# Kernel tuning notes

Hardware: AMD Instinct MI355X
Metric: run time of the kernel (lower is better)

The kernel has to match this reference:

```python
import jax, jax.numpy as jnp
import numpy as np
import math

B, LQ, LK = 4, 512, 512
D_MODEL, NHEAD, NLABELS = 512, 8, 8
D_Q = D_MODEL // NHEAD


def setup_inputs() -> dict:
    key = jax.random.key(0)
    ks = jax.random.split(key, 12)
    xavier = lambda k, shape: jax.random.uniform(
        k, shape, jnp.float32,
        -math.sqrt(6.0 / (shape[0] + shape[1])), math.sqrt(6.0 / (shape[0] + shape[1])))
    return {
        "q": jax.random.normal(ks[0], (B, LQ, D_MODEL), jnp.float32),
        "k": jax.random.normal(ks[1], (B, LK, D_MODEL), jnp.float32),
        "edge_mask": jax.random.randint(ks[2], (B, LQ, LK, NLABELS), 0, 2).astype(jnp.float32),
        "padding_mask": jax.random.randint(ks[3], (B, LQ, LK), 0, 2).astype(jnp.float32),
        "w_q_w": xavier(ks[4], (D_MODEL, D_MODEL)),
        "w_q_b": jnp.zeros((D_MODEL,), jnp.float32),
        "w_k": xavier(ks[5], (D_MODEL, D_MODEL)),
        "w_v": xavier(ks[6], (D_MODEL, D_MODEL)),
        "w_h_w": xavier(ks[7], (D_MODEL, D_MODEL)),
        "w_h_b": jnp.zeros((D_MODEL,), jnp.float32),
        "b_ks": xavier(ks[8], (NLABELS, D_Q)),
        "b_vs": xavier(ks[9], (NLABELS, D_Q)),
    }


def reference(q, k, edge_mask, padding_mask, w_q_w, w_q_b, w_k, w_v, w_h_w, w_h_b, b_ks, b_vs):
    sz_b, len_q, _ = q.shape
    len_k = k.shape[1]
    temp = np.power(D_Q, 0.5).astype(np.float32)

    # projections -> (nhead, B, L, d_q), matching torch permute(2,0,1,3)
    query = (q @ w_q_w.T + w_q_b).reshape(sz_b, len_q, NHEAD, D_Q).transpose(2, 0, 1, 3)
    key = (k @ w_k.T).reshape(sz_b, len_k, NHEAD, D_Q).transpose(2, 0, 1, 3)
    value = (k @ w_v.T).reshape(sz_b, len_k, NHEAD, D_Q).transpose(2, 0, 1, 3)

    # content scores + relation-bias scores
    qk = jnp.einsum('hbqd,hbkd->hbqk', query, key)
    key_rel = jnp.einsum('bqkl,ld->bqkd', edge_mask, b_ks)      # (B,Lq,Lk,d_q)
    qkr = jnp.einsum('hbqd,bqkd->hbqk', query, key_rel)
    output_attention_weights = (qk + qkr) / temp                # pre-mask, as returned by torch

    # mask where no edge label AND padding_mask==1
    relation_mask = (edge_mask.sum(-1) + (1.0 - padding_mask)) == 0  # (B,Lq,Lk)
    rm = relation_mask[None, :, :, :]                                # broadcast over heads
    attn = jnp.where(rm, -jnp.inf, output_attention_weights)
    attn = jax.nn.softmax(attn, axis=-1)
    attn = jnp.where(rm, 0.0, attn)

    # value aggregation: content + relation values
    qv = jnp.einsum('hbqk,hbkd->hbqd', attn, value)
    val_rel = jnp.einsum('bqkl,ld->bqkd', edge_mask, b_vs)
    qvr = jnp.einsum('hbqk,bqkd->hbqd', attn, val_rel)

    out = (qv + qvr).transpose(1, 2, 0, 3).reshape(sz_b, len_q, D_MODEL)
    out = out @ w_h_w.T + w_h_b
    return out, output_attention_weights.reshape(NHEAD * sz_b, len_q, len_k)
```

## Files before the change

kernel.cpp:

```cpp
#include <hip/hip_runtime.h>
#include <math.h>

#define NB 4
#define LQ 512
#define LK 512
#define DM 512
#define NH 8
#define DQ 64
#define NL 8
#define QT 32
#define PSTR 520

typedef short bf16x8 __attribute__((ext_vector_type(8)));
typedef float f32x4 __attribute__((ext_vector_type(4)));

__device__ __forceinline__ unsigned short f2bf(float x) {
    unsigned u = __float_as_uint(x);
    u += 0x7fff + ((u >> 16) & 1);
    return (unsigned short)(u >> 16);
}
__device__ __forceinline__ float bf2f(unsigned x) {
    return __uint_as_float(x << 16);
}
__device__ __forceinline__ void gld16(const void* g, void* l) {
    __builtin_amdgcn_global_load_lds(
        (const __attribute__((address_space(1))) void*)g,
        (__attribute__((address_space(3))) void*)l, 16, 0, 0);
}

__global__ __launch_bounds__(256) void prep_kernel(
        const float* __restrict__ q,  const float* __restrict__ k,
        const float* __restrict__ wq, const float* __restrict__ wk,
        const float* __restrict__ wv, const float* __restrict__ wh,
        const float* __restrict__ em, const float* __restrict__ pad,
        unsigned short* __restrict__ qb,  unsigned short* __restrict__ kb,
        unsigned short* __restrict__ wqb, unsigned short* __restrict__ wkb,
        unsigned short* __restrict__ wvb, unsigned short* __restrict__ whb,
        unsigned short* __restrict__ Pk) {
    const int tid = threadIdx.x;
    const int y = blockIdx.y;
    if (y < 6) {
        const float* s; unsigned short* d; int n;
        switch (y) {
            case 0: s = q;  d = qb;  n = NB * LQ * DM; break;
            case 1: s = k;  d = kb;  n = NB * LK * DM; break;
            case 2: s = wq; d = wqb; n = DM * DM; break;
            case 3: s = wk; d = wkb; n = DM * DM; break;
            case 4: s = wv; d = wvb; n = DM * DM; break;
            default: s = wh; d = whb; n = DM * DM; break;
        }
        const int i = blockIdx.x * 256 + tid;
        if (i * 8 >= n) return;
        const float4* sv = (const float4*)s;
        const float4 a = sv[2 * (size_t)i], b = sv[2 * (size_t)i + 1];
        uint4 o;
        o.x = (unsigned)f2bf(a.x) | ((unsigned)f2bf(a.y) << 16);
        o.y = (unsigned)f2bf(a.z) | ((unsigned)f2bf(a.w) << 16);
        o.z = (unsigned)f2bf(b.x) | ((unsigned)f2bf(b.y) << 16);
        o.w = (unsigned)f2bf(b.z) | ((unsigned)f2bf(b.w) << 16);
        *(uint4*)(d + (size_t)i * 8) = o;
    } else {
        if (blockIdx.x >= 512) return;
        const int row = blockIdx.x * 4 + (tid >> 6);
        const int k0 = (tid & 63) * 8;
        const float* eb = em + ((size_t)row * LK + k0) * NL;
        const float4 pv0 = *(const float4*)(pad + (size_t)row * LK + k0);
        const float4 pv1 = *(const float4*)(pad + (size_t)row * LK + k0 + 4);
        const float pv[8] = {pv0.x, pv0.y, pv0.z, pv0.w, pv1.x, pv1.y, pv1.z, pv1.w};
        unsigned short outv[8];
#pragma unroll
        for (int kk = 0; kk < 8; ++kk) {
            const float4 v0 = *(const float4*)(eb + kk * 8);
            const float4 v1 = *(const float4*)(eb + kk * 8 + 4);
            unsigned b_ = 0;
            b_ |= (v0.x != 0.f) << 0; b_ |= (v0.y != 0.f) << 1;
            b_ |= (v0.z != 0.f) << 2; b_ |= (v0.w != 0.f) << 3;
            b_ |= (v1.x != 0.f) << 4; b_ |= (v1.y != 0.f) << 5;
            b_ |= (v1.z != 0.f) << 6; b_ |= (v1.w != 0.f) << 7;
            b_ |= (pv[kk] != 0.f) << 8;
            outv[kk] = (unsigned short)b_;
        }
        uint4 o;
        o.x = (unsigned)outv[0] | ((unsigned)outv[1] << 16);
        o.y = (unsigned)outv[2] | ((unsigned)outv[3] << 16);
        o.z = (unsigned)outv[4] | ((unsigned)outv[5] << 16);
        o.w = (unsigned)outv[6] | ((unsigned)outv[7] << 16);
        *(uint4*)(Pk + (size_t)row * LK + k0) = o;
    }
}

__device__ __forceinline__ void gemm64core(const unsigned short* __restrict__ Ag, int lda,
                                           const unsigned short* __restrict__ Bg, int ldb,
                                           int K, short* As, short* Bs,
                                           f32x4 (&acc)[2][2]) {
    const int tid = threadIdx.x;
    const int wave = tid >> 6, lane = tid & 63;
    const int quad = lane >> 4, l16 = lane & 15;
    const int wr = wave >> 1, wc = wave & 1;
    for (int k0 = 0; k0 < K; k0 += 32) {
        __syncthreads();
        gld16(Ag + (size_t)(tid >> 2) * lda + k0 + (tid & 3) * 8, (char*)As + wave * 1024);
        gld16(Bg + (size_t)(tid >> 2) * ldb + k0 + (tid & 3) * 8, (char*)Bs + wave * 1024);
        __syncthreads();
        bf16x8 af[2], bf[2];
#pragma unroll
        for (int i = 0; i < 2; ++i)
            af[i] = *(const bf16x8*)&As[(wr * 32 + i * 16 + l16) * 32 + quad * 8];
#pragma unroll
        for (int j = 0; j < 2; ++j)
            bf[j] = *(const bf16x8*)&Bs[(wc * 32 + j * 16 + l16) * 32 + quad * 8];
#pragma unroll
        for (int i = 0; i < 2; ++i)
#pragma unroll
            for (int j = 0; j < 2; ++j)
                acc[i][j] = __builtin_amdgcn_mfma_f32_16x16x32_bf16(af[i], bf[j], acc[i][j], 0, 0, 0);
    }
}

__global__ __launch_bounds__(256) void proj_all(const unsigned short* __restrict__ qb,
                                                const unsigned short* __restrict__ kb,
                                                const unsigned short* __restrict__ wqb,
                                                const unsigned short* __restrict__ wkb,
                                                const unsigned short* __restrict__ wvb,
                                                const float* __restrict__ w_q_b,
                                                unsigned short* __restrict__ Qp,
                                                unsigned short* __restrict__ Kp,
                                                unsigned short* __restrict__ Vt) {
    __shared__ __align__(16) short As[64 * 32];
    __shared__ __align__(16) short Bs[64 * 32];
    const unsigned short* A; const unsigned short* W; const float* bias;
    unsigned short* C; int mode;
    switch (blockIdx.z) {
        case 0:  A = qb; W = wqb; bias = w_q_b;  C = Qp; mode = 0; break;
        case 1:  A = kb; W = wkb; bias = nullptr; C = Kp; mode = 0; break;
        default: A = kb; W = wvb; bias = nullptr; C = Vt; mode = 1; break;
    }
    f32x4 acc[2][2];
    const f32x4 zz = {0.f, 0.f, 0.f, 0.f};
#pragma unroll
    for (int i = 0; i < 2; ++i)
#pragma unroll
        for (int j = 0; j < 2; ++j) acc[i][j] = zz;
    const int m0 = blockIdx.x * 64, n0 = blockIdx.y * 64;
    gemm64core(A + (size_t)m0 * DM, DM, W + (size_t)n0 * DM, DM, DM, As, Bs, acc);
    const int tid = threadIdx.x, wave = tid >> 6, lane = tid & 63;
    const int quad = lane >> 4, l16 = lane & 15;
    const int wr = wave >> 1, wc = wave & 1;
#pragma unroll
    for (int i = 0; i < 2; ++i)
#pragma unroll
        for (int r = 0; r < 4; ++r) {
            const int gm = m0 + wr * 32 + i * 16 + quad * 4 + r;
#pragma unroll
            for (int j = 0; j < 2; ++j) {
                const int gn = n0 + wc * 32 + j * 16 + l16;
                float v = acc[i][j][r];
                if (bias) v += bias[gn];
                if (mode == 0) C[(size_t)gm * DM + gn] = f2bf(v);
                else C[(size_t)(gm >> 9) * (DM * LK) + (size_t)gn * LK + (gm & 511)] = f2bf(v);
            }
        }
}

__global__ __launch_bounds__(512, 4) void attn_fused(
        const unsigned short* __restrict__ Qp,
        const unsigned short* __restrict__ Kp,
        const unsigned short* __restrict__ Vt,
        const unsigned short* __restrict__ Pk,
        const float* __restrict__ b_ks,
        const float* __restrict__ b_vs,
        float* __restrict__ weights,
        unsigned short* __restrict__ Hb) {
    __shared__ __align__(16) short Qs[QT * 64];
    __shared__ __align__(16) short Kc[128 * 64];
    __shared__ __align__(16) short Ps[QT * PSTR];
    __shared__ float svS[QT * NL];
    __shared__ float tS[QT * NL];
    __shared__ float redA[QT * 8];
    __shared__ float redB[QT * 8];

    const int tid = threadIdx.x, wave = tid >> 6, lane = tid & 63;
    const int quad = lane >> 4, l16 = lane & 15;
    const int q0 = blockIdx.x * QT;
    const int z = blockIdx.y, h = z >> 2, b = z & 3;

    if (tid < 256) {
        const int row = tid >> 3, ch = tid & 7;
        gld16(Qp + (size_t)(b * LQ + q0 + row) * DM + h * DQ + ((ch ^ (row & 7)) * 8),
              (char*)Qs + wave * 1024);
    }

    f32x4 acc[4][2];
    const f32x4 zz = {0.f, 0.f, 0.f, 0.f};
#pragma unroll
    for (int c = 0; c < 4; ++c) { acc[c][0] = zz; acc[c][1] = zz; }

    for (int c = 0; c < 4; ++c) {
#pragma unroll
        for (int it = 0; it < 2; ++it) {
            const int e = it * 512 + tid;
            const int kr = e >> 3, ch = e & 7;
            gld16(Kp + (size_t)(b * LK + c * 128 + kr) * DM + h * DQ + ((ch ^ (kr & 7)) * 8),
                  (char*)Kc + it * 8192 + wave * 1024);
        }
        __syncthreads();
#pragma unroll
        for (int kd = 0; kd < 64; kd += 32) {
            const int krow = wave * 16 + l16;
            const int kch = ((kd >> 3) + quad) ^ (krow & 7);
            const bf16x8 bfv = *(const bf16x8*)&Kc[krow * 64 + kch * 8];
#pragma unroll
            for (int i = 0; i < 2; ++i) {
                const int qrow = i * 16 + l16;
                const int qch = ((kd >> 3) + quad) ^ (qrow & 7);
                const bf16x8 afv = *(const bf16x8*)&Qs[qrow * 64 + qch * 8];
                acc[c][i] = __builtin_amdgcn_mfma_f32_16x16x32_bf16(afv, bfv, acc[c][i], 0, 0, 0);
            }
        }
        if (c == 0 && tid < 256) {
            const int row = tid >> 3, l = tid & 7;
            float s = 0.f;
#pragma unroll
            for (int d = 0; d < DQ; ++d) {
                const int ds = ((d >> 3) ^ (row & 7)) * 8 + (d & 7);
                s = fmaf(bf2f((unsigned short)Qs[row * 64 + ds]), b_ks[l * DQ + d], s);
            }
            svS[row * 8 + l] = s;
        }
        __syncthreads();
    }

#pragma unroll
    for (int it = 0; it < 2; ++it) {
        const int e = it * 512 + tid;
        const int dd = e >> 4, ch = e & 15;
        gld16(Vt + (size_t)(b * DM + h * DQ + dd) * LK + ((ch ^ (dd & 15)) * 8),
              (char*)Kc + it * 8192 + wave * 1024);
    }

#pragma unroll
    for (int i = 0; i < 2; ++i)
#pragma unroll
        for (int r = 0; r < 4; ++r) {
            const int row = i * 16 + quad * 4 + r;
            const int gq = q0 + row;
            const f32x4 sv0 = *(const f32x4*)&svS[row * 8];
            const f32x4 sv1 = *(const f32x4*)&svS[row * 8 + 4];
            const unsigned short* prow = Pk + (size_t)(b * LQ + gq) * LK;
            float* wrow = weights + ((size_t)z * LQ + gq) * LK;
            float pm = -__builtin_inff();
#pragma unroll
            for (int c = 0; c < 4; ++c) {
                const int col = c * 128 + wave * 16 + l16;
                const unsigned w_ = prow[col];
                float rel = 0.f;
                rel = fmaf((float)((w_ >> 0) & 1), sv0[0], rel);
                rel = fmaf((float)((w_ >> 1) & 1), sv0[1], rel);
                rel = fmaf((float)((w_ >> 2) & 1), sv0[2], rel);
                rel = fmaf((float)((w_ >> 3) & 1), sv0[3], rel);
                rel = fmaf((float)((w_ >> 4) & 1), sv1[0], rel);
                rel = fmaf((float)((w_ >> 5) & 1), sv1[1], rel);
                rel = fmaf((float)((w_ >> 6) & 1), sv1[2], rel);
                rel = fmaf((float)((w_ >> 7) & 1), sv1[3], rel);
                const float wv = (acc[c][i][r] + rel) * 0.125f;
                wrow[col] = wv;
                const float m = ((w_ & 0x1FFu) == 0x100u) ? -__builtin_inff() : wv;
                acc[c][i][r] = m;
                pm = fmaxf(pm, m);
            }
#pragma unroll
            for (int o = 1; o < 16; o <<= 1) pm = fmaxf(pm, __shfl_xor(pm, o, 64));
            float ps = 0.f;
#pragma unroll
            for (int c = 0; c < 4; ++c) {
                const float e = __expf(acc[c][i][r] - pm);
                acc[c][i][r] = e;
                ps += e;
            }
#pragma unroll
            for (int o = 1; o < 16; o <<= 1) ps += __shfl_xor(ps, o, 64);
            if (l16 == 0) { redA[row * 8 + wave] = pm; redB[row * 8 + wave] = ps; }
        }
    __syncthreads();

#pragma unroll
    for (int i = 0; i < 2; ++i)
#pragma unroll
        for (int r = 0; r < 4; ++r) {
            const int row = i * 16 + quad * 4 + r;
            const f32x4 pa = *(const f32x4*)&redA[row * 8];
            const f32x4 pb = *(const f32x4*)&redA[row * 8 + 4];
            const f32x4 sa = *(const f32x4*)&redB[row * 8];
            const f32x4 sb = *(const f32x4*)&redB[row * 8 + 4];
            const float M = fmaxf(fmaxf(fmaxf(pa[0], pa[1]), fmaxf(pa[2], pa[3])),
                                  fmaxf(fmaxf(pb[0], pb[1]), fmaxf(pb[2], pb[3])));
            const float S = sa[0] * __expf(pa[0] - M) + sa[1] * __expf(pa[1] - M)
                          + sa[2] * __expf(pa[2] - M) + sa[3] * __expf(pa[3] - M)
                          + sb[0] * __expf(pb[0] - M) + sb[1] * __expf(pb[1] - M)
                          + sb[2] * __expf(pb[2] - M) + sb[3] * __expf(pb[3] - M);
            const float own = redA[row * 8 + wave];
            const float alpha = __expf(own - M) / S;
#pragma unroll
            for (int c = 0; c < 4; ++c) {
                const int col = c * 128 + wave * 16 + l16;
                Ps[row * PSTR + col] = (short)f2bf(acc[c][i][r] * alpha);
            }
        }
    __syncthreads();

    {
        const int row = tid >> 4, l = (tid >> 1) & 7, half = tid & 1;
        const uint4* pw = (const uint4*)(Pk + (size_t)(b * LQ + q0 + row) * LK + half * 256);
        const uint4* aw = (const uint4*)&Ps[row * PSTR + half * 256];
        float tv = 0.f;
#pragma unroll 4
        for (int kk = 0; kk < 32; ++kk) {
            const uint4 wb = pw[kk];
            const uint4 av = aw[kk];
            const unsigned w4[4] = {wb.x, wb.y, wb.z, wb.w};
            const unsigned a4[4] = {av.x, av.y, av.z, av.w};
#pragma unroll
            for (int u = 0; u < 4; ++u) {
                tv += ((w4[u] >> l) & 1)        ? bf2f(a4[u] & 0xffffu) : 0.f;
                tv += ((w4[u] >> (16 + l)) & 1) ? bf2f(a4[u] >> 16)     : 0.f;
            }
        }
        tv += __shfl_xor(tv, 1, 64);
        if (half == 0) tS[row * 8 + l] = tv;
    }

    f32x4 oacc = zz;
    const int mi = wave & 1, ni = wave >> 1;
    for (int vc = 0; vc < 4; ++vc) {
        if (vc > 0) {
            __syncthreads();
#pragma unroll
            for (int it = 0; it < 2; ++it) {
                const int e = it * 512 + tid;
                const int dd = e >> 4, ch = e & 15;
                gld16(Vt + (size_t)(b * DM + h * DQ + dd) * LK + vc * 128 + ((ch ^ (dd & 15)) * 8),
                      (char*)Kc + it * 8192 + wave * 1024);
            }
            __syncthreads();
        }
#pragma unroll
        for (int kd = 0; kd < 128; kd += 32) {
            const int vrow = ni * 16 + l16;
            const int vch = ((kd >> 3) + quad) ^ (vrow & 15);
            const bf16x8 afv = *(const bf16x8*)&Ps[(mi * 16 + l16) * PSTR + vc * 128 + kd + quad * 8];
            const bf16x8 bfv = *(const bf16x8*)&Kc[vrow * 128 + vch * 8];
            oacc = __builtin_amdgcn_mfma_f32_16x16x32_bf16(afv, bfv, oacc, 0, 0, 0);
        }
    }

    const int gd = ni * 16 + l16;
    float bvv[NL];
#pragma unroll
    for (int l = 0; l < NL; ++l) bvv[l] = b_vs[l * DQ + gd];
#pragma unroll
    for (int r = 0; r < 4; ++r) {
        const int row = mi * 16 + quad * 4 + r;
        const float* tp = &tS[row * 8];
        float o = oacc[r];
#pragma unroll
        for (int l = 0; l < NL; ++l) o = fmaf(tp[l], bvv[l], o);
        Hb[(size_t)(b * LQ + q0 + row) * DM + h * DQ + gd] = f2bf(o);
    }
}

__global__ __launch_bounds__(256) void outproj_mfma(const unsigned short* __restrict__ Hb,
                                                    const unsigned short* __restrict__ whb,
                                                    const float* __restrict__ bias,
                                                    float* __restrict__ C) {
    __shared__ __align__(16) short As[64 * 32];
    __shared__ __align__(16) short Bs[64 * 32];
    f32x4 acc[2][2];
    const f32x4 zz = {0.f, 0.f, 0.f, 0.f};
#pragma unroll
    for (int i = 0; i < 2; ++i)
#pragma unroll
        for (int j = 0; j < 2; ++j) acc[i][j] = zz;
    const int m0 = blockIdx.x * 64, n0 = blockIdx.y * 64;
    gemm64core(Hb + (size_t)m0 * DM, DM, whb + (size_t)n0 * DM, DM, DM, As, Bs, acc);
    const int tid = threadIdx.x, wave = tid >> 6, lane = tid & 63;
    const int quad = lane >> 4, l16 = lane & 15;
    const int wr = wave >> 1, wc = wave & 1;
#pragma unroll
    for (int i = 0; i < 2; ++i)
#pragma unroll
        for (int r = 0; r < 4; ++r) {
            const int gm = m0 + wr * 32 + i * 16 + quad * 4 + r;
#pragma unroll
            for (int j = 0; j < 2; ++j) {
                const int gn = n0 + wc * 32 + j * 16 + l16;
                C[(size_t)gm * DM + gn] = acc[i][j][r] + bias[gn];
            }
        }
}

extern "C" void kernel_launch(void* const* d_in, const int* in_sizes, int n_in,
                              void* d_out, int out_size, void* d_ws, size_t ws_size,
                              hipStream_t stream) {
    const float* q     = (const float*)d_in[0];
    const float* k     = (const float*)d_in[1];
    const float* em    = (const float*)d_in[2];
    const float* pad   = (const float*)d_in[3];
    const float* w_q_w = (const float*)d_in[4];
    const float* w_q_b = (const float*)d_in[5];
    const float* w_k   = (const float*)d_in[6];
    const float* w_v   = (const float*)d_in[7];
    const float* w_h_w = (const float*)d_in[8];
    const float* w_h_b = (const float*)d_in[9];
    const float* b_ks  = (const float*)d_in[10];
    const float* b_vs  = (const float*)d_in[11];

    float* out     = (float*)d_out;
    float* weights = out + (size_t)NB * LQ * DM;

    char* ws = (char*)d_ws;
    unsigned short* qb  = (unsigned short*)(ws + 0);
    unsigned short* kb  = (unsigned short*)(ws + 2097152);
    unsigned short* wqb = (unsigned short*)(ws + 4194304);
    unsigned short* wkb = (unsigned short*)(ws + 4718592);
    unsigned short* wvb = (unsigned short*)(ws + 5242880);
    unsigned short* whb = (unsigned short*)(ws + 5767168);
    unsigned short* Qp  = (unsigned short*)(ws + 6291456);
    unsigned short* Kp  = (unsigned short*)(ws + 8388608);
    unsigned short* Vt  = (unsigned short*)(ws + 10485760);
    unsigned short* Hb  = (unsigned short*)(ws + 12582912);
    unsigned short* Pk  = (unsigned short*)(ws + 14680064);

    prep_kernel<<<dim3(1024, 7), 256, 0, stream>>>(q, k, w_q_w, w_k, w_v, w_h_w,
                                                   em, pad, qb, kb, wqb, wkb, wvb, whb, Pk);
    proj_all<<<dim3(32, 8, 3), 256, 0, stream>>>(qb, kb, wqb, wkb, wvb, w_q_b, Qp, Kp, Vt);
    attn_fused<<<dim3(LQ / QT, 32), 512, 0, stream>>>(Qp, Kp, Vt, Pk, b_ks, b_vs, weights, Hb);
    outproj_mfma<<<dim3(32, 8), 256, 0, stream>>>(Hb, whb, w_h_b, out);
}
```

Measured before the change: 169.9 us.

## Use LUT for relation bias, fp16 P/V with packed masked sums, hoist Q fragments

Replaces the per-element 8-FMA relation-bias computation with two lookups into a per-row 16-entry table built in shared memory. Switches the probability and V^T storage from bf16 to fp16 so the PV MFMA uses the f16 instruction. This lets the label-weighted probability sums use packed half-precision multiplies with bit masks. It also computes svS from global Q with all threads and keeps Q fragments in registers across K chunks. The risk is precision loss from fp16 partial accumulation, and extra LDS traffic from the table.

```diff
diff --git a/kernel.cpp b/kernel.cpp
--- a/kernel.cpp
+++ b/kernel.cpp
@@ -12,6 +12,8 @@
 #define PSTR 520
 
 typedef short bf16x8 __attribute__((ext_vector_type(8)));
+typedef _Float16 f16x8 __attribute__((ext_vector_type(8)));
+typedef _Float16 f16x2 __attribute__((ext_vector_type(2)));
 typedef float f32x4 __attribute__((ext_vector_type(4)));
 
 __device__ __forceinline__ unsigned short f2bf(float x) {
@@ -21,6 +23,10 @@
 }
 __device__ __forceinline__ float bf2f(unsigned x) {
     return __uint_as_float(x << 16);
+}
+__device__ __forceinline__ unsigned short f2h(float x) {
+    _Float16 h = (_Float16)x;
+    return __builtin_bit_cast(unsigned short, h);
 }
 __device__ __forceinline__ void gld16(const void* g, void* l) {
     __builtin_amdgcn_global_load_lds(
@@ -157,7 +163,7 @@
                 float v = acc[i][j][r];
                 if (bias) v += bias[gn];
                 if (mode == 0) C[(size_t)gm * DM + gn] = f2bf(v);
-                else C[(size_t)(gm >> 9) * (DM * LK) + (size_t)gn * LK + (gm & 511)] = f2bf(v);
+                else C[(size_t)(gm >> 9) * (DM * LK) + (size_t)gn * LK + (gm & 511)] = f2h(v);
             }
         }
 }
@@ -175,6 +181,7 @@
     __shared__ __align__(16) short Kc[128 * 64];
     __shared__ __align__(16) short Ps[QT * PSTR];
     __shared__ float svS[QT * NL];
+    __shared__ float lutS[QT * 32];
     __shared__ float tS[QT * NL];
     __shared__ float redA[QT * 8];
     __shared__ float redB[QT * 8];
@@ -190,10 +197,27 @@
               (char*)Qs + wave * 1024);
     }
 
+    {
+        const int row = tid >> 4, l = (tid >> 1) & 7, half = tid & 1;
+        const unsigned short* qrow = Qp + (size_t)(b * LQ + q0 + row) * DM + h * DQ + half * 32;
+        const float* bk = b_ks + l * DQ + half * 32;
+        float s = 0.f;
+#pragma unroll
+        for (int d0 = 0; d0 < 32; d0 += 8) {
+            const bf16x8 qv = *(const bf16x8*)&qrow[d0];
+#pragma unroll
+            for (int j = 0; j < 8; ++j)
+                s = fmaf(bf2f((unsigned short)qv[j]), bk[d0 + j], s);
+        }
+        s += __shfl_xor(s, 1, 64);
+        if (half == 0) svS[row * 8 + l] = s;
+    }
+
     f32x4 acc[4][2];
     const f32x4 zz = {0.f, 0.f, 0.f, 0.f};
 #pragma unroll
     for (int c = 0; c < 4; ++c) { acc[c][0] = zz; acc[c][1] = zz; }
+    bf16x8 qf[2][2];
 
     for (int c = 0; c < 4; ++c) {
 #pragma unroll
@@ -204,28 +228,34 @@
                   (char*)Kc + it * 8192 + wave * 1024);
         }
         __syncthreads();
-#pragma unroll
-        for (int kd = 0; kd < 64; kd += 32) {
+        if (c == 0) {
+#pragma unroll
+            for (int i = 0; i < 2; ++i)
+#pragma unroll
+                for (int kdi = 0; kdi < 2; ++kdi)
+                    qf[i][kdi] = *(const bf16x8*)&Qs[(i * 16 + l16) * 64
+                                                     + (((kdi * 4) + quad) ^ (l16 & 7)) * 8];
+        }
+#pragma unroll
+        for (int kdi = 0; kdi < 2; ++kdi) {
             const int krow = wave * 16 + l16;
-            const int kch = ((kd >> 3) + quad) ^ (krow & 7);
+            const int kch = (kdi * 4 + quad) ^ (krow & 7);
             const bf16x8 bfv = *(const bf16x8*)&Kc[krow * 64 + kch * 8];
 #pragma unroll
-            for (int i = 0; i < 2; ++i) {
-                const int qrow = i * 16 + l16;
-                const int qch = ((kd >> 3) + quad) ^ (qrow & 7);
-                const bf16x8 afv = *(const bf16x8*)&Qs[qrow * 64 + qch * 8];
-                acc[c][i] = __builtin_amdgcn_mfma_f32_16x16x32_bf16(afv, bfv, acc[c][i], 0, 0, 0);
-            }
-        }
-        if (c == 0 && tid < 256) {
-            const int row = tid >> 3, l = tid & 7;
-            float s = 0.f;
-#pragma unroll
-            for (int d = 0; d < DQ; ++d) {
-                const int ds = ((d >> 3) ^ (row & 7)) * 8 + (d & 7);
-                s = fmaf(bf2f((unsigned short)Qs[row * 64 + ds]), b_ks[l * DQ + d], s);
-            }
-            svS[row * 8 + l] = s;
+            for (int i = 0; i < 2; ++i)
+                acc[c][i] = __builtin_amdgcn_mfma_f32_16x16x32_bf16(qf[i][kdi], bfv, acc[c][i], 0, 0, 0);
+        }
+        if (c == 0) {
+            for (int e = tid; e < QT * 32; e += 512) {
+                const int row = e >> 5, idx = e & 31;
+                const float* s = &svS[row * 8 + ((idx & 16) ? 4 : 0)];
+                float v = 0.f;
+                v += (idx & 1) ? s[0] : 0.f;
+                v += (idx & 2) ? s[1] : 0.f;
+                v += (idx & 4) ? s[2] : 0.f;
+                v += (idx & 8) ? s[3] : 0.f;
+                lutS[e] = v;
+            }
         }
         __syncthreads();
     }
@@ -244,8 +274,7 @@
         for (int r = 0; r < 4; ++r) {
             const int row = i * 16 + quad * 4 + r;
             const int gq = q0 + row;
-            const f32x4 sv0 = *(const f32x4*)&svS[row * 8];
-            const f32x4 sv1 = *(const f32x4*)&svS[row * 8 + 4];
+            const float* lrow = &lutS[row * 32];
             const unsigned short* prow = Pk + (size_t)(b * LQ + gq) * LK;
             float* wrow = weights + ((size_t)z * LQ + gq) * LK;
             float pm = -__builtin_inff();
@@ -253,15 +282,7 @@
             for (int c = 0; c < 4; ++c) {
                 const int col = c * 128 + wave * 16 + l16;
                 const unsigned w_ = prow[col];
-                float rel = 0.f;
-                rel = fmaf((float)((w_ >> 0) & 1), sv0[0], rel);
-                rel = fmaf((float)((w_ >> 1) & 1), sv0[1], rel);
-                rel = fmaf((float)((w_ >> 2) & 1), sv0[2], rel);
-                rel = fmaf((float)((w_ >> 3) & 1), sv0[3], rel);
-                rel = fmaf((float)((w_ >> 4) & 1), sv1[0], rel);
-                rel = fmaf((float)((w_ >> 5) & 1), sv1[1], rel);
-                rel = fmaf((float)((w_ >> 6) & 1), sv1[2], rel);
-                rel = fmaf((float)((w_ >> 7) & 1), sv1[3], rel);
+                const float rel = lrow[w_ & 15u] + lrow[16 + ((w_ >> 4) & 15u)];
                 const float wv = (acc[c][i][r] + rel) * 0.125f;
                 wrow[col] = wv;
                 const float m = ((w_ & 0x1FFu) == 0x100u) ? -__builtin_inff() : wv;
@@ -303,7 +324,7 @@
 #pragma unroll
             for (int c = 0; c < 4; ++c) {
                 const int col = c * 128 + wave * 16 + l16;
-                Ps[row * PSTR + col] = (short)f2bf(acc[c][i][r] * alpha);
+                Ps[row * PSTR + col] = (short)f2h(acc[c][i][r] * alpha);
             }
         }
     __syncthreads();
@@ -319,11 +340,14 @@
             const uint4 av = aw[kk];
             const unsigned w4[4] = {wb.x, wb.y, wb.z, wb.w};
             const unsigned a4[4] = {av.x, av.y, av.z, av.w};
+            f16x2 hacc = {(_Float16)0.f, (_Float16)0.f};
 #pragma unroll
             for (int u = 0; u < 4; ++u) {
-                tv += ((w4[u] >> l) & 1)        ? bf2f(a4[u] & 0xffffu) : 0.f;
-                tv += ((w4[u] >> (16 + l)) & 1) ? bf2f(a4[u] >> 16)     : 0.f;
-            }
+                const unsigned bits = (w4[u] >> l) & 0x10001u;
+                const unsigned msk = bits * 0x3c00u;
+                hacc += __builtin_bit_cast(f16x2, a4[u]) * __builtin_bit_cast(f16x2, msk);
+            }
+            tv += (float)hacc[0] + (float)hacc[1];
         }
         tv += __shfl_xor(tv, 1, 64);
         if (half == 0) tS[row * 8 + l] = tv;
@@ -347,9 +371,9 @@
         for (int kd = 0; kd < 128; kd += 32) {
             const int vrow = ni * 16 + l16;
             const int vch = ((kd >> 3) + quad) ^ (vrow & 15);
-            const bf16x8 afv = *(const bf16x8*)&Ps[(mi * 16 + l16) * PSTR + vc * 128 + kd + quad * 8];
-            const bf16x8 bfv = *(const bf16x8*)&Kc[vrow * 128 + vch * 8];
-            oacc = __builtin_amdgcn_mfma_f32_16x16x32_bf16(afv, bfv, oacc, 0, 0, 0);
+            const f16x8 afv = *(const f16x8*)&Ps[(mi * 16 + l16) * PSTR + vc * 128 + kd + quad * 8];
+            const f16x8 bfv = *(const f16x8*)&Kc[vrow * 128 + vch * 8];
+            oacc = __builtin_amdgcn_mfma_f32_16x16x32_f16(afv, bfv, oacc, 0, 0, 0);
         }
     }
 
```

After: 168.1 us. About the same (-1.1%).
